# Kernel tuning notes

Hardware: AMD Instinct MI355X
Metric: run time of the kernel (lower is better)

## Reference

```python
import jax, jax.numpy as jnp
import numpy as np

WS = 16      # window_size
FW = 1       # focal_window -> 3x3 grid of focal windows
FF = 2       # focal_factor (avg-pool for non-center windows)
NH = 8       # num_heads

_OFFSETS = [(di, dj) for di in range(-FW, FW + 1) for dj in range(-FW, FW + 1)]
# tokens contributed by each focal window (center keeps full res, neighbors pooled)
_COUNTS = np.array([WS * WS if (di == 0 and dj == 0) else (WS // FF) ** 2 for di, dj in _OFFSETS])
# center window gets zero bias, peripheral windows get -position_bias (intent of add_focal_bias)
_MULTS = np.array([0.0 if (di == 0 and dj == 0) else -1.0 for di, dj in _OFFSETS], dtype=np.float32)


def _gather_focal(x):
    """x: (B,H,W,C) -> (B*nW, kv_len, C) focal key/value tokens per window."""
    B, H, W, C = x.shape
    nH, nWg = H // WS, W // WS
    xp = jnp.pad(x, ((0, 0), (WS, WS), (WS, WS), (0, 0)), mode='reflect')
    # padded window grid: (B, nH+2, nWg+2, WS, WS, C)
    g = xp.reshape(B, nH + 2, WS, nWg + 2, WS, C).transpose(0, 1, 3, 2, 4, 5)
    parts = []
    for di, dj in _OFFSETS:
        w = g[:, 1 + di:1 + di + nH, 1 + dj:1 + dj + nWg]  # (B,nH,nWg,WS,WS,C)
        if di == 0 and dj == 0:
            t = w.reshape(B, nH, nWg, WS * WS, C)
        else:
            p = WS // FF  # avg_pool2d(kernel=stride=FF)
            t = w.reshape(B, nH, nWg, p, FF, p, FF, C).mean(axis=(4, 6)).reshape(B, nH, nWg, p * p, C)
        parts.append(t)
    kv = jnp.concatenate(parts, axis=3)  # (B,nH,nWg,kv_len,C)
    return kv.reshape(B * nH * nWg, -1, C)


def _bias_tokens(position_bias):
    # (NH, 9) -> (NH, kv_len): per-focal-window bias broadcast over its tokens
    scaled = position_bias * jnp.asarray(_MULTS)[None, :]
    return jnp.repeat(scaled, _COUNTS, axis=1)


def reference(x, Wq, bq, Wk, bk, Wv, bv, Wo, bo, position_bias):
    B, H, W, C = x.shape
    hd = C // NH
    scale = hd ** -0.5
    nH, nWg = H // WS, W // WS
    # window partition: (B*nW, WS*WS, C)
    xw = x.reshape(B, nH, WS, nWg, WS, C).transpose(0, 1, 3, 2, 4, 5).reshape(-1, WS * WS, C)
    kv = _gather_focal(x)  # (B*nW, kv_len, C)
    q = (xw @ Wq + bq).reshape(-1, WS * WS, NH, hd).transpose(0, 2, 1, 3)
    k = (kv @ Wk + bk).reshape(kv.shape[0], -1, NH, hd).transpose(0, 2, 1, 3)
    v = (kv @ Wv + bv).reshape(kv.shape[0], -1, NH, hd).transpose(0, 2, 1, 3)
    attn = jnp.einsum('whqd,whkd->whqk', q, k) * scale
    attn = attn + _bias_tokens(position_bias)[None, :, None, :]
    attn = jax.nn.softmax(attn, axis=-1)
    out = jnp.einsum('whqk,whkd->whqd', attn, v).transpose(0, 2, 1, 3).reshape(-1, WS * WS, C)
    out = out @ Wo + bo
    # window reverse
    out = out.reshape(B, nH, nWg, WS, WS, C).transpose(0, 1, 3, 2, 4, 5).reshape(B, H, W, C)
    return out


def setup_inputs() -> dict:
    key = jax.random.key(0)
    ks = jax.random.split(key, 10)
    D = 384
    w = lambda k: jax.random.normal(k, (D, D), dtype=jnp.float32) * 0.02
    b = lambda k: jax.random.normal(k, (D,), dtype=jnp.float32) * 0.02
    return {
        'x': jax.random.normal(ks[0], (2, 128, 128, D), dtype=jnp.float32),
        'Wq': w(ks[1]), 'bq': b(ks[2]),
        'Wk': w(ks[3]), 'bk': b(ks[4]),
        'Wv': w(ks[5]), 'bv': b(ks[6]),
        'Wo': w(ks[7]), 'bo': b(ks[8]),
        'position_bias': jax.random.normal(ks[9], (NH, 9), dtype=jnp.float32) * 0.02,
    }
```

## Files before the change

kernel.cpp:

```cpp
#include <hip/hip_runtime.h>
#include <hip/hip_bf16.h>

#define NTOK 32768
#define LOG2E 1.4426950408889634f

typedef __attribute__((ext_vector_type(8))) short bf16x8;
typedef __attribute__((ext_vector_type(4))) float f32x4;

__device__ __forceinline__ float bf2f(unsigned short u) {
  return __uint_as_float(((unsigned int)u) << 16);
}
__device__ __forceinline__ unsigned short f2bf(float f) {
  union { __hip_bfloat16 h; unsigned short u; } cv;
  cv.h = __float2bfloat16(f);
  return cv.u;
}
__device__ __forceinline__ unsigned cvt_pk_bf16(float lo, float hi) {
  unsigned r;
  asm("v_cvt_pk_bf16_f32 %0, %1, %2" : "=v"(r) : "v"(lo), "v"(hi));
  return r;
}
__device__ __forceinline__ float fast_exp2(float x) {
#if __has_builtin(__builtin_amdgcn_exp2f)
  return __builtin_amdgcn_exp2f(x);
#else
  return exp2f(x);
#endif
}

__device__ __forceinline__ void gload16(const void* g, void* l) {
  __builtin_amdgcn_global_load_lds(
      (const __attribute__((address_space(1))) unsigned int*)(unsigned long long)g,
      (__attribute__((address_space(3))) unsigned int*)(unsigned long long)l, 16, 0, 0);
}

__global__ __launch_bounds__(256) void convert_x(const float* __restrict__ x,
                                                 unsigned short* __restrict__ xb) {
  const int i = (blockIdx.x * 256 + threadIdx.x) * 8;
  float4 a = *(const float4*)(x + i);
  float4 b = *(const float4*)(x + i + 4);
  *(ushort4*)(xb + i)     = make_ushort4(f2bf(a.x), f2bf(a.y), f2bf(a.z), f2bf(a.w));
  *(ushort4*)(xb + i + 4) = make_ushort4(f2bf(b.x), f2bf(b.y), f2bf(b.z), f2bf(b.w));
}

__global__ __launch_bounds__(256) void transpose_w(const float* __restrict__ Wq,
                                                   const float* __restrict__ Wk,
                                                   const float* __restrict__ Wv,
                                                   const float* __restrict__ Wo,
                                                   unsigned short* __restrict__ Wt) {
  __shared__ float tile[32][33];
  const int wsel = blockIdx.z;
  const float* W = (wsel == 0) ? Wq : (wsel == 1) ? Wk : (wsel == 2) ? Wv : Wo;
  unsigned short* out = Wt + (size_t)wsel * 147456;
  const int k0 = blockIdx.x * 32, n0 = blockIdx.y * 32;
  const int r = threadIdx.x >> 3, c4 = (threadIdx.x & 7) * 4;
  float4 v = *(const float4*)&W[(size_t)(k0 + r) * 384 + n0 + c4];
  tile[r][c4 + 0] = v.x; tile[r][c4 + 1] = v.y; tile[r][c4 + 2] = v.z; tile[r][c4 + 3] = v.w;
  __syncthreads();
  ushort4 o = make_ushort4(f2bf(tile[c4 + 0][r]), f2bf(tile[c4 + 1][r]),
                           f2bf(tile[c4 + 2][r]), f2bf(tile[c4 + 3][r]));
  *(ushort4*)&out[(size_t)(n0 + r) * 384 + k0 + c4] = o;
}

__global__ __launch_bounds__(192) void pool_kernel(const unsigned short* __restrict__ xb,
                                                   unsigned short* __restrict__ P) {
  const int unit = blockIdx.x * 192 + threadIdx.x;
  const int cell = unit / 48;
  const int c8 = (unit - cell * 48) * 8;
  const int b = cell / 6400;
  const int rem = cell - b * 6400;
  const int p0 = rem / 80, p1 = rem - p0 * 80;
  const int i0 = 2 * p0 - 16, i1 = i0 + 1;
  const int j0 = 2 * p1 - 16, j1 = j0 + 1;
  const int r0 = i0 < 0 ? -i0 : (i0 > 127 ? 254 - i0 : i0);
  const int r1 = i1 < 0 ? -i1 : (i1 > 127 ? 254 - i1 : i1);
  const int c0 = j0 < 0 ? -j0 : (j0 > 127 ? 254 - j0 : j0);
  const int c1 = j1 < 0 ? -j1 : (j1 > 127 ? 254 - j1 : j1);
  uint4 u00 = *(const uint4*)(xb + ((size_t)((b * 128 + r0) * 128 + c0)) * 384 + c8);
  uint4 u01 = *(const uint4*)(xb + ((size_t)((b * 128 + r0) * 128 + c1)) * 384 + c8);
  uint4 u10 = *(const uint4*)(xb + ((size_t)((b * 128 + r1) * 128 + c0)) * 384 + c8);
  uint4 u11 = *(const uint4*)(xb + ((size_t)((b * 128 + r1) * 128 + c1)) * 384 + c8);
  const unsigned short* a0 = (const unsigned short*)&u00;
  const unsigned short* a1 = (const unsigned short*)&u01;
  const unsigned short* a2 = (const unsigned short*)&u10;
  const unsigned short* a3 = (const unsigned short*)&u11;
  unsigned short o[8];
  #pragma unroll
  for (int j = 0; j < 8; ++j)
    o[j] = f2bf(0.25f * (bf2f(a0[j]) + bf2f(a1[j]) + bf2f(a2[j]) + bf2f(a3[j])));
  uint4 ov;
  unsigned short* op = (unsigned short*)&ov;
  #pragma unroll
  for (int j = 0; j < 8; ++j) op[j] = o[j];
  *(uint4*)(P + (size_t)cell * 384 + c8) = ov;
}

__global__ __launch_bounds__(256) void mfma_proj_fused(
    const unsigned short* __restrict__ xb, const unsigned short* __restrict__ P,
    const unsigned short* __restrict__ Wt,
    const float* __restrict__ bq, const float* __restrict__ bk, const float* __restrict__ bv,
    unsigned short* __restrict__ Qb, unsigned short* __restrict__ Kcat,
    unsigned short* __restrict__ Vcat) {
  const int bid = blockIdx.x;
  const unsigned short* X;
  int wsel, colblk, yy; size_t off;
  if (bid < 2304) {
    const int xx = bid % 9; yy = bid / 9;
    X = xb; wsel = xx / 3; colblk = xx % 3; off = 0;
  } else {
    const int r = bid - 2304; const int xx = r % 6; yy = r / 6;
    X = P; wsel = 1 + xx / 3; colblk = xx % 3; off = (size_t)NTOK * 384;
  }
  const float* bias = (wsel == 0) ? bq : (wsel == 1) ? bk : bv;
  unsigned short* Y = ((wsel == 0) ? Qb : (wsel == 1) ? Kcat : Vcat) + off;
  const unsigned short* Wm = Wt + (size_t)wsel * 147456;
  const int n0 = colblk * 128;
  const int m0 = yy * 128;

  __shared__ __attribute__((aligned(16))) unsigned short As[3][128 * 32];
  __shared__ __attribute__((aligned(16))) unsigned short Bs[3][128 * 32];
  const int t = threadIdx.x;
  const int w = t >> 6, l = t & 63, l15 = l & 15, g = l >> 4;
  const int wm = w >> 1, wn = w & 1;
  const int srow = (w * 2) * 16 + (l >> 2), srow2 = (w * 2 + 1) * 16 + (l >> 2);
  const int skc = (l & 3) * 8;

  f32x4 acc[4][4];
  #pragma unroll
  for (int i = 0; i < 4; ++i)
    #pragma unroll
    for (int j = 0; j < 4; ++j) acc[i][j] = {0.f, 0.f, 0.f, 0.f};

  #pragma unroll
  for (int pt = 0; pt < 2; ++pt) {
    const int k0 = pt * 32;
    gload16(X  + (size_t)(m0 + srow)  * 384 + k0 + skc, &As[pt][(w * 2)     * 512]);
    gload16(X  + (size_t)(m0 + srow2) * 384 + k0 + skc, &As[pt][(w * 2 + 1) * 512]);
    gload16(Wm + (size_t)(n0 + srow)  * 384 + k0 + skc, &Bs[pt][(w * 2)     * 512]);
    gload16(Wm + (size_t)(n0 + srow2) * 384 + k0 + skc, &Bs[pt][(w * 2 + 1) * 512]);
  }

  for (int kt = 0; kt < 12; ++kt) {
    if (kt < 11) asm volatile("s_waitcnt vmcnt(4)" ::: "memory");
    else         asm volatile("s_waitcnt vmcnt(0)" ::: "memory");
    __builtin_amdgcn_s_barrier();
    __builtin_amdgcn_sched_barrier(0);
    if (kt < 10) {
      const int k0 = (kt + 2) * 32;
      const int bnext = (kt + 2) % 3;
      gload16(X  + (size_t)(m0 + srow)  * 384 + k0 + skc, &As[bnext][(w * 2)     * 512]);
      gload16(X  + (size_t)(m0 + srow2) * 384 + k0 + skc, &As[bnext][(w * 2 + 1) * 512]);
      gload16(Wm + (size_t)(n0 + srow)  * 384 + k0 + skc, &Bs[bnext][(w * 2)     * 512]);
      gload16(Wm + (size_t)(n0 + srow2) * 384 + k0 + skc, &Bs[bnext][(w * 2 + 1) * 512]);
    }
    const int cur = kt % 3;
    bf16x8 af[4], bfr[4];
    #pragma unroll
    for (int mi = 0; mi < 4; ++mi)
      af[mi] = *(const bf16x8*)(&As[cur][(wm * 64 + mi * 16 + l15) * 32 + g * 8]);
    #pragma unroll
    for (int nj = 0; nj < 4; ++nj)
      bfr[nj] = *(const bf16x8*)(&Bs[cur][(wn * 64 + nj * 16 + l15) * 32 + g * 8]);
    #pragma unroll
    for (int mi = 0; mi < 4; ++mi)
      #pragma unroll
      for (int nj = 0; nj < 4; ++nj)
        acc[mi][nj] = __builtin_amdgcn_mfma_f32_16x16x32_bf16(af[mi], bfr[nj], acc[mi][nj], 0, 0, 0);
  }

  float bv4[4];
  #pragma unroll
  for (int nj = 0; nj < 4; ++nj) bv4[nj] = bias[n0 + wn * 64 + nj * 16 + l15];
  #pragma unroll
  for (int mi = 0; mi < 4; ++mi)
    #pragma unroll
    for (int nj = 0; nj < 4; ++nj)
      #pragma unroll
      for (int r = 0; r < 4; ++r) {
        const size_t row = m0 + wm * 64 + mi * 16 + g * 4 + r;
        const size_t col = n0 + wn * 64 + nj * 16 + l15;
        Y[row * 384 + col] = f2bf(acc[mi][nj][r] + bv4[nj]);
      }
}

__global__ __launch_bounds__(256) void mfma_proj_out(const unsigned short* __restrict__ X,
                                                     const unsigned short* __restrict__ Wm,
                                                     const float* __restrict__ bias,
                                                     float* __restrict__ Y) {
  const int n0 = blockIdx.x * 128, m0 = blockIdx.y * 128;
  __shared__ __attribute__((aligned(16))) unsigned short As[3][128 * 32];
  __shared__ __attribute__((aligned(16))) unsigned short Bs[3][128 * 32];
  const int t = threadIdx.x;
  const int w = t >> 6, l = t & 63, l15 = l & 15, g = l >> 4;
  const int wm = w >> 1, wn = w & 1;
  const int srow = (w * 2) * 16 + (l >> 2), srow2 = (w * 2 + 1) * 16 + (l >> 2);
  const int skc = (l & 3) * 8;

  f32x4 acc[4][4];
  #pragma unroll
  for (int i = 0; i < 4; ++i)
    #pragma unroll
    for (int j = 0; j < 4; ++j) acc[i][j] = {0.f, 0.f, 0.f, 0.f};

  #pragma unroll
  for (int pt = 0; pt < 2; ++pt) {
    const int k0 = pt * 32;
    gload16(X  + (size_t)(m0 + srow)  * 384 + k0 + skc, &As[pt][(w * 2)     * 512]);
    gload16(X  + (size_t)(m0 + srow2) * 384 + k0 + skc, &As[pt][(w * 2 + 1) * 512]);
    gload16(Wm + (size_t)(n0 + srow)  * 384 + k0 + skc, &Bs[pt][(w * 2)     * 512]);
    gload16(Wm + (size_t)(n0 + srow2) * 384 + k0 + skc, &Bs[pt][(w * 2 + 1) * 512]);
  }

  for (int kt = 0; kt < 12; ++kt) {
    if (kt < 11) asm volatile("s_waitcnt vmcnt(4)" ::: "memory");
    else         asm volatile("s_waitcnt vmcnt(0)" ::: "memory");
    __builtin_amdgcn_s_barrier();
    __builtin_amdgcn_sched_barrier(0);
    if (kt < 10) {
      const int k0 = (kt + 2) * 32;
      const int bnext = (kt + 2) % 3;
      gload16(X  + (size_t)(m0 + srow)  * 384 + k0 + skc, &As[bnext][(w * 2)     * 512]);
      gload16(X  + (size_t)(m0 + srow2) * 384 + k0 + skc, &As[bnext][(w * 2 + 1) * 512]);
      gload16(Wm + (size_t)(n0 + srow)  * 384 + k0 + skc, &Bs[bnext][(w * 2)     * 512]);
      gload16(Wm + (size_t)(n0 + srow2) * 384 + k0 + skc, &Bs[bnext][(w * 2 + 1) * 512]);
    }
    const int cur = kt % 3;
    bf16x8 af[4], bfr[4];
    #pragma unroll
    for (int mi = 0; mi < 4; ++mi)
      af[mi] = *(const bf16x8*)(&As[cur][(wm * 64 + mi * 16 + l15) * 32 + g * 8]);
    #pragma unroll
    for (int nj = 0; nj < 4; ++nj)
      bfr[nj] = *(const bf16x8*)(&Bs[cur][(wn * 64 + nj * 16 + l15) * 32 + g * 8]);
    #pragma unroll
    for (int mi = 0; mi < 4; ++mi)
      #pragma unroll
      for (int nj = 0; nj < 4; ++nj)
        acc[mi][nj] = __builtin_amdgcn_mfma_f32_16x16x32_bf16(af[mi], bfr[nj], acc[mi][nj], 0, 0, 0);
  }

  float bv4[4];
  #pragma unroll
  for (int nj = 0; nj < 4; ++nj) bv4[nj] = bias[n0 + wn * 64 + nj * 16 + l15];
  #pragma unroll
  for (int mi = 0; mi < 4; ++mi)
    #pragma unroll
    for (int nj = 0; nj < 4; ++nj)
      #pragma unroll
      for (int r = 0; r < 4; ++r) {
        const size_t row = m0 + wm * 64 + mi * 16 + g * 4 + r;
        const size_t col = n0 + wn * 64 + nj * 16 + l15;
        Y[row * 384 + col] = acc[mi][nj][r] + bv4[nj];
      }
}

__global__ __launch_bounds__(256) void attn_mfma(const unsigned short* __restrict__ Qg,
                                                 const unsigned short* __restrict__ Kc,
                                                 const unsigned short* __restrict__ Vc,
                                                 const float* __restrict__ pb,
                                                 unsigned short* __restrict__ AttO) {
  __shared__ unsigned short kvb[768];
  __shared__ float tb2s[12];
  __shared__ __attribute__((aligned(16))) unsigned short Ks[2][3072];
  __shared__ __attribute__((aligned(16))) unsigned short Vt[2][64 * 68];

  const int t = threadIdx.x;
  const int bid = blockIdx.x;
  const int head = (bid >> 3) & 7;
  const int win  = (bid & 7) + 8 * (bid >> 6);
  const int b = win >> 6, wrem = win & 63, wi = wrem >> 3, wj = wrem & 7;
  const int w = t >> 6, l = t & 63, l15 = l & 15, g = l >> 4;
  const int hb = head * 48;

  for (int j = t; j < 768; j += 256) {
    int o, within;
    if (j < 256)      { o = j >> 6;               within = j & 63; }
    else if (j < 512) { o = 4;                    within = j - 256; }
    else              { o = 5 + ((j - 512) >> 6); within = j & 63; }
    int tok;
    if (o == 4) {
      int r = within >> 4, c = within & 15;
      tok = (b * 128 + wi * 16 + r) * 128 + wj * 16 + c;
    } else {
      int di = o / 3 - 1, dj = o - (o / 3) * 3 - 1;
      int t0 = within >> 3, t1 = within & 7;
      int p0 = 8 * (1 + di + wi) + t0, p1 = 8 * (1 + dj + wj) + t1;
      tok = NTOK + (b * 80 + p0) * 80 + p1;
    }
    kvb[j] = (unsigned short)tok;
  }
  if (t < 12) {
    int o = (t < 4) ? t : ((t < 8) ? 4 : t - 3);
    tb2s[t] = (o == 4) ? 0.0f : (-pb[head * 9 + o] * LOG2E);
  }
  for (int idx = t; idx < 2 * 16 * 68; idx += 256) {
    const int bu = idx / 1088, rem = idx - bu * 1088;
    const int rr = rem / 68, cc = rem - rr * 68;
    Vt[bu][(48 + rr) * 68 + cc] = (rr == 0) ? 0x3F80 : 0;
  }

  const float SCALE2 = 0.14433756729740643f * LOG2E;
  const bf16x8 z8 = {0, 0, 0, 0, 0, 0, 0, 0};

  bf16x8 qf[4][2];
  #pragma unroll
  for (int nf = 0; nf < 4; ++nf) {
    const int tok = ((b * 128 + wi * 16 + w * 4 + nf) * 128 + wj * 16 + l15);
    const unsigned short* qp = Qg + (size_t)tok * 384 + hb;
    qf[nf][0] = *(const bf16x8*)(qp + g * 8);
    qf[nf][1] = (g < 2) ? *(const bf16x8*)(qp + 32 + g * 8) : z8;
  }

  f32x4 Oacc[4][4];
  #pragma unroll
  for (int mo = 0; mo < 4; ++mo)
    #pragma unroll
    for (int nf = 0; nf < 4; ++nf) Oacc[mo][nf] = {0.f, 0.f, 0.f, 0.f};

  __syncthreads();

  uint4 va0, va1;
  {
    const int kvb0 = (int)kvb[l] * 384 + hb;
    gload16(Kc + kvb0 + w * 8, &Ks[0][w * 512]);
    if (w < 2) gload16(Kc + kvb0 + (4 + w) * 8, &Ks[0][(4 + w) * 512]);
    va0 = *(const uint4*)(Vc + kvb0 + w * 8);
    va1 = (w < 2) ? *(const uint4*)(Vc + kvb0 + (4 + w) * 8) : make_uint4(0, 0, 0, 0);
  }

  for (int T = 0; T < 12; ++T) {
    const int buf = T & 1;
    asm volatile("s_waitcnt vmcnt(0)" ::: "memory");
    {
      const unsigned short* u0 = (const unsigned short*)&va0;
      #pragma unroll
      for (int s = 0; s < 8; ++s) Vt[buf][(w * 8 + s) * 68 + l] = u0[s];
      if (w < 2) {
        const unsigned short* u1 = (const unsigned short*)&va1;
        #pragma unroll
        for (int s = 0; s < 8; ++s) Vt[buf][((4 + w) * 8 + s) * 68 + l] = u1[s];
      }
    }
    __syncthreads();
    if (T < 11) {
      const int kvb2 = (int)kvb[(T + 1) * 64 + l] * 384 + hb;
      gload16(Kc + kvb2 + w * 8, &Ks[buf ^ 1][w * 512]);
      if (w < 2) gload16(Kc + kvb2 + (4 + w) * 8, &Ks[buf ^ 1][(4 + w) * 512]);
      va0 = *(const uint4*)(Vc + kvb2 + w * 8);
      if (w < 2) va1 = *(const uint4*)(Vc + kvb2 + (4 + w) * 8);
    }

    const float tb = tb2s[T];
    #pragma unroll
    for (int h = 0; h < 2; ++h) {
      bf16x8 ka[2][2];
      #pragma unroll
      for (int mi = 0; mi < 2; ++mi) {
        const int krow = h * 32 + mi * 16 + l15;
        ka[mi][0] = *(const bf16x8*)&Ks[buf][g * 512 + krow * 8];
        ka[mi][1] = *(const bf16x8*)&Ks[buf][(4 + (g & 1)) * 512 + krow * 8];
      }
      f32x4 sf[2][4];
      #pragma unroll
      for (int mi = 0; mi < 2; ++mi)
        #pragma unroll
        for (int nf = 0; nf < 4; ++nf) sf[mi][nf] = {0.f, 0.f, 0.f, 0.f};
      __builtin_amdgcn_s_setprio(1);
      #pragma unroll
      for (int mi = 0; mi < 2; ++mi)
        #pragma unroll
        for (int nf = 0; nf < 4; ++nf) {
          sf[mi][nf] = __builtin_amdgcn_mfma_f32_16x16x32_bf16(ka[mi][0], qf[nf][0], sf[mi][nf], 0, 0, 0);
          sf[mi][nf] = __builtin_amdgcn_mfma_f32_16x16x32_bf16(ka[mi][1], qf[nf][1], sf[mi][nf], 0, 0, 0);
        }
      __builtin_amdgcn_s_setprio(0);

      bf16x8 pbf[4];
      #pragma unroll
      for (int nf = 0; nf < 4; ++nf) {
        float p[8];
        #pragma unroll
        for (int r = 0; r < 4; ++r) {
          p[r]     = fast_exp2(fmaf(sf[0][nf][r], SCALE2, tb));
          p[4 + r] = fast_exp2(fmaf(sf[1][nf][r], SCALE2, tb));
        }
        unsigned a0 = cvt_pk_bf16(p[0], p[1]);
        unsigned a1 = cvt_pk_bf16(p[2], p[3]);
        unsigned b0 = cvt_pk_bf16(p[4], p[5]);
        unsigned b1 = cvt_pk_bf16(p[6], p[7]);
        asm("v_permlane32_swap_b32 %0, %1" : "+v"(a0), "+v"(b0));
        asm("v_permlane32_swap_b32 %0, %1" : "+v"(a1), "+v"(b1));
        asm("v_permlane16_swap_b32 %0, %1" : "+v"(a0), "+v"(b0));
        asm("v_permlane16_swap_b32 %0, %1" : "+v"(a1), "+v"(b1));
        union { bf16x8 v; unsigned u[4]; } cv;
        cv.u[0] = a0; cv.u[1] = a1; cv.u[2] = b0; cv.u[3] = b1;
        pbf[nf] = cv.v;
      }

      #pragma unroll
      for (int mo = 0; mo < 4; ++mo) {
        const unsigned short* vp = &Vt[buf][(mo * 16 + l15) * 68 + h * 32 + g * 8];
        union { bf16x8 v; ushort4 u[2]; } cv;
        cv.u[0] = *(const ushort4*)vp;
        cv.u[1] = *(const ushort4*)(vp + 4);
        bf16x8 va = cv.v;
        __builtin_amdgcn_s_setprio(1);
        #pragma unroll
        for (int nf = 0; nf < 4; ++nf)
          Oacc[mo][nf] = __builtin_amdgcn_mfma_f32_16x16x32_bf16(va, pbf[nf], Oacc[mo][nf], 0, 0, 0);
        __builtin_amdgcn_s_setprio(0);
      }
    }
  }

  #pragma unroll
  for (int nf = 0; nf < 4; ++nf) {
    const float denom = __shfl(Oacc[3][nf][0], l15, 64);
    const float inv = 1.0f / denom;
    const int tok = ((b * 128 + wi * 16 + w * 4 + nf) * 128 + wj * 16 + l15);
    unsigned short* op = AttO + (size_t)tok * 384 + hb;
    #pragma unroll
    for (int mo = 0; mo < 3; ++mo) {
      uint2 u;
      u.x = cvt_pk_bf16(Oacc[mo][nf][0] * inv, Oacc[mo][nf][1] * inv);
      u.y = cvt_pk_bf16(Oacc[mo][nf][2] * inv, Oacc[mo][nf][3] * inv);
      *(uint2*)(op + mo * 16 + g * 4) = u;
    }
  }
}

extern "C" void kernel_launch(void* const* d_in, const int* in_sizes, int n_in,
                              void* d_out, int out_size, void* d_ws, size_t ws_size,
                              hipStream_t stream) {
  const float* x  = (const float*)d_in[0];
  const float* Wq = (const float*)d_in[1];
  const float* bq = (const float*)d_in[2];
  const float* Wk = (const float*)d_in[3];
  const float* bk = (const float*)d_in[4];
  const float* Wv = (const float*)d_in[5];
  const float* bv = (const float*)d_in[6];
  const float* Wo = (const float*)d_in[7];
  const float* bo = (const float*)d_in[8];
  const float* pb = (const float*)d_in[9];

  char* ws = (char*)d_ws;
  unsigned short* Wt   = (unsigned short*)(ws);
  unsigned short* P    = (unsigned short*)(ws + 1179648ull);
  unsigned short* Kcat = (unsigned short*)(ws + 11010048ull);
  unsigned short* Vcat = (unsigned short*)(ws + 46006272ull);
  unsigned short* xb   = (unsigned short*)(ws + 81002496ull);
  unsigned short* AttO = xb;
  unsigned short* Qb   = (unsigned short*)d_out;

  convert_x<<<6144, 256, 0, stream>>>(x, xb);
  pool_kernel<<<3200, 192, 0, stream>>>(xb, P);
  transpose_w<<<dim3(12, 12, 4), 256, 0, stream>>>(Wq, Wk, Wv, Wo, Wt);
  mfma_proj_fused<<<2904, 256, 0, stream>>>(xb, P, Wt, bq, bk, bv, Qb, Kcat, Vcat);
  attn_mfma<<<1024, 256, 0, stream>>>(Qb, Kcat, Vcat, pb, AttO);
  mfma_proj_out<<<dim3(3, 256), 256, 0, stream>>>(AttO, Wt + 3 * 147456, bo, (float*)d_out);
}
```

Before: 186.7 us.

## Use 256x128 tiles with 512-thread blocks for projection GEMMs

Replaces the two 128x128-tile projection GEMM kernels with one templated kernel using 256-row tiles and 8 waves per block. This halves the number of blocks and the reloads of weight tiles, improving operand reuse per block. The attention kernel's block-to-(head, window) mapping also changes to head-major order. The larger shared memory footprint may reduce occupancy.

Result: no change. 190.3 us (+1.9%).

```diff
diff --git a/kernel.cpp b/kernel.cpp
--- a/kernel.cpp
+++ b/kernel.cpp
@@ -95,35 +95,49 @@
   *(uint4*)(P + (size_t)cell * 384 + c8) = ov;
 }
 
-__global__ __launch_bounds__(256) void mfma_proj_fused(
+template<int FUSED>
+__global__ __launch_bounds__(512) void mfma_proj256(
     const unsigned short* __restrict__ xb, const unsigned short* __restrict__ P,
     const unsigned short* __restrict__ Wt,
     const float* __restrict__ bq, const float* __restrict__ bk, const float* __restrict__ bv,
     unsigned short* __restrict__ Qb, unsigned short* __restrict__ Kcat,
-    unsigned short* __restrict__ Vcat) {
+    unsigned short* __restrict__ Vcat, float* __restrict__ Yf) {
   const int bid = blockIdx.x;
   const unsigned short* X;
-  int wsel, colblk, yy; size_t off;
-  if (bid < 2304) {
-    const int xx = bid % 9; yy = bid / 9;
-    X = xb; wsel = xx / 3; colblk = xx % 3; off = 0;
+  const unsigned short* Wm;
+  const float* bias;
+  unsigned short* Yb = nullptr;
+  float* Yout = nullptr;
+  int n0, m0;
+  if (FUSED) {
+    int wsel, colblk, yy; size_t off;
+    if (bid < 1152) {
+      const int xx = bid % 9; yy = bid / 9;
+      X = xb; wsel = xx / 3; colblk = xx % 3; off = 0;
+    } else {
+      const int r = bid - 1152; const int xx = r % 6; yy = r / 6;
+      X = P; wsel = 1 + xx / 3; colblk = xx % 3; off = (size_t)NTOK * 384;
+    }
+    bias = (wsel == 0) ? bq : (wsel == 1) ? bk : bv;
+    Yb = ((wsel == 0) ? Qb : (wsel == 1) ? Kcat : Vcat) + off;
+    Wm = Wt + (size_t)wsel * 147456;
+    n0 = colblk * 128; m0 = yy * 256;
   } else {
-    const int r = bid - 2304; const int xx = r % 6; yy = r / 6;
-    X = P; wsel = 1 + xx / 3; colblk = xx % 3; off = (size_t)NTOK * 384;
-  }
-  const float* bias = (wsel == 0) ? bq : (wsel == 1) ? bk : bv;
-  unsigned short* Y = ((wsel == 0) ? Qb : (wsel == 1) ? Kcat : Vcat) + off;
-  const unsigned short* Wm = Wt + (size_t)wsel * 147456;
-  const int n0 = colblk * 128;
-  const int m0 = yy * 128;
-
-  __shared__ __attribute__((aligned(16))) unsigned short As[3][128 * 32];
+    X = xb;
+    Wm = Wt + 3ull * 147456;
+    bias = bq;
+    Yout = Yf;
+    n0 = (bid % 3) * 128; m0 = (bid / 3) * 256;
+  }
+
+  __shared__ __attribute__((aligned(16))) unsigned short As[3][256 * 32];
   __shared__ __attribute__((aligned(16))) unsigned short Bs[3][128 * 32];
   const int t = threadIdx.x;
   const int w = t >> 6, l = t & 63, l15 = l & 15, g = l >> 4;
-  const int wm = w >> 1, wn = w & 1;
-  const int srow = (w * 2) * 16 + (l >> 2), srow2 = (w * 2 + 1) * 16 + (l >> 2);
-  const int skc = (l & 3) * 8;
+  const int wm = w & 3, wn = w >> 2;
+
+  const int ua0 = w * 128 + l, ua1 = w * 128 + 64 + l;
+  const int ub  = w * 64 + l;
 
   f32x4 acc[4][4];
   #pragma unroll
@@ -134,24 +148,22 @@
   #pragma unroll
   for (int pt = 0; pt < 2; ++pt) {
     const int k0 = pt * 32;
-    gload16(X  + (size_t)(m0 + srow)  * 384 + k0 + skc, &As[pt][(w * 2)     * 512]);
-    gload16(X  + (size_t)(m0 + srow2) * 384 + k0 + skc, &As[pt][(w * 2 + 1) * 512]);
-    gload16(Wm + (size_t)(n0 + srow)  * 384 + k0 + skc, &Bs[pt][(w * 2)     * 512]);
-    gload16(Wm + (size_t)(n0 + srow2) * 384 + k0 + skc, &Bs[pt][(w * 2 + 1) * 512]);
+    gload16(X  + (size_t)(m0 + (ua0 >> 2)) * 384 + k0 + (ua0 & 3) * 8, &As[pt][(w * 128) * 8]);
+    gload16(X  + (size_t)(m0 + (ua1 >> 2)) * 384 + k0 + (ua1 & 3) * 8, &As[pt][(w * 128 + 64) * 8]);
+    gload16(Wm + (size_t)(n0 + (ub  >> 2)) * 384 + k0 + (ub  & 3) * 8, &Bs[pt][(w * 64) * 8]);
   }
 
   for (int kt = 0; kt < 12; ++kt) {
-    if (kt < 11) asm volatile("s_waitcnt vmcnt(4)" ::: "memory");
+    if (kt < 11) asm volatile("s_waitcnt vmcnt(3)" ::: "memory");
     else         asm volatile("s_waitcnt vmcnt(0)" ::: "memory");
     __builtin_amdgcn_s_barrier();
     __builtin_amdgcn_sched_barrier(0);
     if (kt < 10) {
       const int k0 = (kt + 2) * 32;
-      const int bnext = (kt + 2) % 3;
-      gload16(X  + (size_t)(m0 + srow)  * 384 + k0 + skc, &As[bnext][(w * 2)     * 512]);
-      gload16(X  + (size_t)(m0 + srow2) * 384 + k0 + skc, &As[bnext][(w * 2 + 1) * 512]);
-      gload16(Wm + (size_t)(n0 + srow)  * 384 + k0 + skc, &Bs[bnext][(w * 2)     * 512]);
-      gload16(Wm + (size_t)(n0 + srow2) * 384 + k0 + skc, &Bs[bnext][(w * 2 + 1) * 512]);
+      const int bn = (kt + 2) % 3;
+      gload16(X  + (size_t)(m0 + (ua0 >> 2)) * 384 + k0 + (ua0 & 3) * 8, &As[bn][(w * 128) * 8]);
+      gload16(X  + (size_t)(m0 + (ua1 >> 2)) * 384 + k0 + (ua1 & 3) * 8, &As[bn][(w * 128 + 64) * 8]);
+      gload16(Wm + (size_t)(n0 + (ub  >> 2)) * 384 + k0 + (ub  & 3) * 8, &Bs[bn][(w * 64) * 8]);
     }
     const int cur = kt % 3;
     bf16x8 af[4], bfr[4];
@@ -179,78 +191,8 @@
       for (int r = 0; r < 4; ++r) {
         const size_t row = m0 + wm * 64 + mi * 16 + g * 4 + r;
         const size_t col = n0 + wn * 64 + nj * 16 + l15;
-        Y[row * 384 + col] = f2bf(acc[mi][nj][r] + bv4[nj]);
-      }
-}
-
-__global__ __launch_bounds__(256) void mfma_proj_out(const unsigned short* __restrict__ X,
-                                                     const unsigned short* __restrict__ Wm,
-                                                     const float* __restrict__ bias,
-                                                     float* __restrict__ Y) {
-  const int n0 = blockIdx.x * 128, m0 = blockIdx.y * 128;
-  __shared__ __attribute__((aligned(16))) unsigned short As[3][128 * 32];
-  __shared__ __attribute__((aligned(16))) unsigned short Bs[3][128 * 32];
-  const int t = threadIdx.x;
-  const int w = t >> 6, l = t & 63, l15 = l & 15, g = l >> 4;
-  const int wm = w >> 1, wn = w & 1;
-  const int srow = (w * 2) * 16 + (l >> 2), srow2 = (w * 2 + 1) * 16 + (l >> 2);
-  const int skc = (l & 3) * 8;
-
-  f32x4 acc[4][4];
-  #pragma unroll
-  for (int i = 0; i < 4; ++i)
-    #pragma unroll
-    for (int j = 0; j < 4; ++j) acc[i][j] = {0.f, 0.f, 0.f, 0.f};
-
-  #pragma unroll
-  for (int pt = 0; pt < 2; ++pt) {
-    const int k0 = pt * 32;
-    gload16(X  + (size_t)(m0 + srow)  * 384 + k0 + skc, &As[pt][(w * 2)     * 512]);
-    gload16(X  + (size_t)(m0 + srow2) * 384 + k0 + skc, &As[pt][(w * 2 + 1) * 512]);
-    gload16(Wm + (size_t)(n0 + srow)  * 384 + k0 + skc, &Bs[pt][(w * 2)     * 512]);
-    gload16(Wm + (size_t)(n0 + srow2) * 384 + k0 + skc, &Bs[pt][(w * 2 + 1) * 512]);
-  }
-
-  for (int kt = 0; kt < 12; ++kt) {
-    if (kt < 11) asm volatile("s_waitcnt vmcnt(4)" ::: "memory");
-    else         asm volatile("s_waitcnt vmcnt(0)" ::: "memory");
-    __builtin_amdgcn_s_barrier();
-    __builtin_amdgcn_sched_barrier(0);
-    if (kt < 10) {
-      const int k0 = (kt + 2) * 32;
-      const int bnext = (kt + 2) % 3;
-      gload16(X  + (size_t)(m0 + srow)  * 384 + k0 + skc, &As[bnext][(w * 2)     * 512]);
-      gload16(X  + (size_t)(m0 + srow2) * 384 + k0 + skc, &As[bnext][(w * 2 + 1) * 512]);
-      gload16(Wm + (size_t)(n0 + srow)  * 384 + k0 + skc, &Bs[bnext][(w * 2)     * 512]);
-      gload16(Wm + (size_t)(n0 + srow2) * 384 + k0 + skc, &Bs[bnext][(w * 2 + 1) * 512]);
-    }
-    const int cur = kt % 3;
-    bf16x8 af[4], bfr[4];
-    #pragma unroll
-    for (int mi = 0; mi < 4; ++mi)
-      af[mi] = *(const bf16x8*)(&As[cur][(wm * 64 + mi * 16 + l15) * 32 + g * 8]);
-    #pragma unroll
-    for (int nj = 0; nj < 4; ++nj)
-      bfr[nj] = *(const bf16x8*)(&Bs[cur][(wn * 64 + nj * 16 + l15) * 32 + g * 8]);
-    #pragma unroll
-    for (int mi = 0; mi < 4; ++mi)
-      #pragma unroll
-      for (int nj = 0; nj < 4; ++nj)
-        acc[mi][nj] = __builtin_amdgcn_mfma_f32_16x16x32_bf16(af[mi], bfr[nj], acc[mi][nj], 0, 0, 0);
-  }
-
-  float bv4[4];
-  #pragma unroll
-  for (int nj = 0; nj < 4; ++nj) bv4[nj] = bias[n0 + wn * 64 + nj * 16 + l15];
-  #pragma unroll
-  for (int mi = 0; mi < 4; ++mi)
-    #pragma unroll
-    for (int nj = 0; nj < 4; ++nj)
-      #pragma unroll
-      for (int r = 0; r < 4; ++r) {
-        const size_t row = m0 + wm * 64 + mi * 16 + g * 4 + r;
-        const size_t col = n0 + wn * 64 + nj * 16 + l15;
-        Y[row * 384 + col] = acc[mi][nj][r] + bv4[nj];
+        if (FUSED) Yb[row * 384 + col] = f2bf(acc[mi][nj][r] + bv4[nj]);
+        else       Yout[row * 384 + col] = acc[mi][nj][r] + bv4[nj];
       }
 }
 
@@ -265,9 +207,7 @@
   __shared__ __attribute__((aligned(16))) unsigned short Vt[2][64 * 68];
 
   const int t = threadIdx.x;
-  const int bid = blockIdx.x;
-  const int head = (bid >> 3) & 7;
-  const int win  = (bid & 7) + 8 * (bid >> 6);
+  const int head = blockIdx.x >> 7, win = blockIdx.x & 127;
   const int b = win >> 6, wrem = win & 63, wi = wrem >> 3, wj = wrem & 7;
   const int w = t >> 6, l = t & 63, l15 = l & 15, g = l >> 4;
   const int hb = head * 48;
@@ -455,7 +395,8 @@
   convert_x<<<6144, 256, 0, stream>>>(x, xb);
   pool_kernel<<<3200, 192, 0, stream>>>(xb, P);
   transpose_w<<<dim3(12, 12, 4), 256, 0, stream>>>(Wq, Wk, Wv, Wo, Wt);
-  mfma_proj_fused<<<2904, 256, 0, stream>>>(xb, P, Wt, bq, bk, bv, Qb, Kcat, Vcat);
+  mfma_proj256<1><<<1452, 512, 0, stream>>>(xb, P, Wt, bq, bk, bv, Qb, Kcat, Vcat, nullptr);
   attn_mfma<<<1024, 256, 0, stream>>>(Qb, Kcat, Vcat, pb, AttO);
-  mfma_proj_out<<<dim3(3, 256), 256, 0, stream>>>(AttO, Wt + 3 * 147456, bo, (float*)d_out);
-}
+  mfma_proj256<0><<<384, 512, 0, stream>>>(AttO, P, Wt, bo, nullptr, nullptr,
+                                           nullptr, nullptr, nullptr, (float*)d_out);
+}
```
